# Kernel tuning notes

Hardware: AMD Instinct MI355X
Metric: run time of the kernel (lower is better)

The kernel has to match this reference:

```python
import jax, jax.numpy as jnp
import numpy as np

SIGMA_DIS = 3.0
MAX_LABELS = 33  # label ids in [0, 32]; 0 = background, 1..32 = kernels


def setup_inputs() -> dict:
    key = jax.random.key(0)
    k1, k2 = jax.random.split(key)
    B, C, H, W = 8, 4, 896, 896
    pred = jax.random.normal(k1, (B, C, H, W), dtype=jnp.float32)
    kernels_mask = jnp.ones((B, H, W), dtype=jnp.float32)
    labels = jax.random.randint(k2, (B, H, W), 0, MAX_LABELS, dtype=jnp.int32)
    return {
        "pred_similarities": pred,
        "kernels_mask": kernels_mask,
        "kernel_mask_ndi_labels": labels,
    }


def _disc_loss(pred, labels, sigma):
    # pred: [B, C, H, W], labels: [B, H, W] int
    B, C = pred.shape[0], pred.shape[1]
    p = pred.reshape(B, C, -1)        # [B, C, N]
    lab = labels.reshape(B, -1)       # [B, N]

    # Masks for distinct labels are disjoint, so for a = pred*mask_i/|K_i|,
    # b = pred*mask_j/|K_j|:  ||a - b||_F^2 = s_i + s_j where
    # s_k = sum_{pixels in K_k} sum_c pred^2 / |K_k|^2.
    sq = jnp.sum(p * p, axis=1)       # [B, N]

    def seg(x, l):
        return jax.ops.segment_sum(x, l, num_segments=MAX_LABELS)

    card = jax.vmap(seg)(jnp.ones_like(sq), lab)   # [B, L] pixel counts
    ssq = jax.vmap(seg)(sq, lab)                   # [B, L] sum of squares
    safe_card = jnp.where(card > 0, card, 1.0)
    s = ssq / (safe_card * safe_card)              # [B, L]

    nk = jnp.max(lab, axis=1)                      # [B] num_kernels per image
    ks = jnp.arange(MAX_LABELS)
    valid = (ks[None, :] >= 1) & (ks[None, :] <= nk[:, None]) & (card > 0)  # [B, L]

    # all unordered pairs i < j of valid labels
    pair_mask = (
        valid[:, :, None] & valid[:, None, :] & (ks[:, None] < ks[None, :])[None]
    )  # [B, L, L]
    S = s[:, :, None] + s[:, None, :]
    S_safe = jnp.where(pair_mask, S, 1.0)          # keep sqrt grads finite
    # NOTE: original torch.max(norm, 0)[0] on a 0-d tensor is a dim-reduction
    # over a size-1 view and is an identity, NOT a clamp; replicated faithfully.
    d = sigma - jnp.sqrt(S_safe)
    term = jnp.log(d * d + 1.0)
    per_b = jnp.sum(jnp.where(pair_mask, term, 0.0), axis=(1, 2))  # [B]

    nk_f = nk.astype(per_b.dtype)
    denom = jnp.where(nk > 1, nk_f * (nk_f - 1.0), 1.0)
    loss_b = jnp.where(nk > 1, per_b / denom, 0.0)
    return jnp.sum(loss_b)


def reference(pred_similarities, kernels_mask, kernel_mask_ndi_labels):
    # kernels_mask is reshaped but never used by the original forward math.
    return _disc_loss(pred_similarities, kernel_mask_ndi_labels, SIGMA_DIS)
```

## Files before the change

### kernel.cpp

```cpp
#include <hip/hip_runtime.h>

#define MAXL 33
#define PB 128
#define TPB 128

__global__ __launch_bounds__(TPB, 2) void seg_hist_kernel(
    const float* __restrict__ pred, const int* __restrict__ labels,
    float* __restrict__ partial, int N) {
  const int b = blockIdx.y;
  const int ng = N >> 2;
  __shared__ float sumh[TPB * MAXL];
  __shared__ unsigned cnth[TPB * MAXL];
  __shared__ float xred[2][2][MAXL];
  const int tid = threadIdx.x;

  float* sh = &sumh[tid * MAXL];
  unsigned* ch = &cnth[tid * MAXL];
#pragma unroll
  for (int i = 0; i < MAXL; ++i) {
    sh[i] = 0.f;
    ch[i] = 0u;
  }

  const float4* p = reinterpret_cast<const float4*>(pred) + (size_t)b * 4 * ng;
  const int4* lb = reinterpret_cast<const int4*>(labels) + (size_t)b * ng;
  const int STRIDE = PB * TPB;

  int g = blockIdx.x * TPB + tid;
  float4 c0 = p[g], c1 = p[g + ng], c2 = p[g + 2 * ng], c3 = p[g + 3 * ng];
  int4 l = lb[g];

  while (true) {
    const int gn = g + STRIDE;
    const bool more = gn < ng;
    float4 n0, n1, n2, n3;
    int4 nl;
    if (more) {
      n0 = p[gn];
      n1 = p[gn + ng];
      n2 = p[gn + 2 * ng];
      n3 = p[gn + 3 * ng];
      nl = lb[gn];
    }

    float s0 = c0.x * c0.x + c1.x * c1.x + c2.x * c2.x + c3.x * c3.x;
    float s1 = c0.y * c0.y + c1.y * c1.y + c2.y * c2.y + c3.y * c3.y;
    float s2 = c0.z * c0.z + c1.z * c1.z + c2.z * c2.z + c3.z * c3.z;
    float s3 = c0.w * c0.w + c1.w * c1.w + c2.w * c2.w + c3.w * c3.w;

    const bool e01 = l.x == l.y, e02 = l.x == l.z, e03 = l.x == l.w;
    const bool e12 = l.y == l.z, e13 = l.y == l.w, e23 = l.z == l.w;
    const float w1 = s1 + (e01 ? s0 : 0.f);
    const float w2 = s2 + (e12 ? s1 : 0.f) + (e02 ? s0 : 0.f);
    const float w3 =
        s3 + (e23 ? s2 : 0.f) + (e13 ? s1 : 0.f) + (e03 ? s0 : 0.f);
    const unsigned m1 = 1u + (unsigned)e01;
    const unsigned m2 = 1u + (unsigned)e12 + (unsigned)e02;
    const unsigned m3 = 1u + (unsigned)e23 + (unsigned)e13 + (unsigned)e03;

    const float r0 = sh[l.x], r1 = sh[l.y], r2 = sh[l.z], r3 = sh[l.w];
    const unsigned q0 = ch[l.x], q1 = ch[l.y], q2 = ch[l.z], q3 = ch[l.w];
    sh[l.x] = r0 + s0;
    sh[l.y] = r1 + w1;
    sh[l.z] = r2 + w2;
    sh[l.w] = r3 + w3;
    ch[l.x] = q0 + 1u;
    ch[l.y] = q1 + m1;
    ch[l.z] = q2 + m2;
    ch[l.w] = q3 + m3;

    if (!more) break;
    c0 = n0;
    c1 = n1;
    c2 = n2;
    c3 = n3;
    l = nl;
    g = gn;
  }
  __syncthreads();

  const int wave = tid >> 6;
  const int lane = tid & 63;
  if (lane < MAXL) {
    float fs = 0.f;
    unsigned fc = 0u;
#pragma unroll 8
    for (int u = 0; u < 64; ++u) {
      fs += sumh[(wave * 64 + u) * MAXL + lane];
      fc += cnth[(wave * 64 + u) * MAXL + lane];
    }
    xred[wave][0][lane] = fs;
    xred[wave][1][lane] = (float)fc;
  }
  __syncthreads();
  if (tid < MAXL) {
    partial[(size_t)(b * 2 * MAXL + tid) * PB + blockIdx.x] =
        xred[0][0][tid] + xred[1][0][tid];
    partial[(size_t)(b * 2 * MAXL + MAXL + tid) * PB + blockIdx.x] =
        xred[0][1][tid] + xred[1][1][tid];
  }
}

__global__ __launch_bounds__(512) void reduce_finalize_kernel(
    const float* __restrict__ partial, float* __restrict__ out) {
  __shared__ float red[8 * 2 * MAXL];
  __shared__ float s_val[8 * MAXL];
  __shared__ float s_flag[8 * MAXL];
  __shared__ float s_invden[8];
  __shared__ float s_part[8];
  const int tid = threadIdx.x;
  const int wave = tid >> 6;
  const int lane = tid & 63;

  {
    int slot = tid;
    const float4* row =
        reinterpret_cast<const float4*>(partial) + (size_t)slot * (PB / 4);
    float a0 = 0.f, a1 = 0.f;
#pragma unroll 8
    for (int u = 0; u < PB / 4; u += 2) {
      float4 x = row[u], y = row[u + 1];
      a0 += x.x + x.y + x.z + x.w;
      a1 += y.x + y.y + y.z + y.w;
    }
    if (slot < 8 * 2 * MAXL) red[slot] = a0 + a1;
  }
  if (tid < 8 * 2 * MAXL - 512) {
    int slot = 512 + tid;
    const float4* row =
        reinterpret_cast<const float4*>(partial) + (size_t)slot * (PB / 4);
    float a0 = 0.f, a1 = 0.f;
#pragma unroll 8
    for (int u = 0; u < PB / 4; u += 2) {
      float4 x = row[u], y = row[u + 1];
      a0 += x.x + x.y + x.z + x.w;
      a1 += y.x + y.y + y.z + y.w;
    }
    red[slot] = a0 + a1;
  }
  __syncthreads();

  for (int i = tid; i < 8 * MAXL; i += 512) {
    int b = i / MAXL, l = i - b * MAXL;
    float cnt = red[b * 2 * MAXL + MAXL + l];
    float ssq = red[b * 2 * MAXL + l];
    float safe = cnt > 0.f ? cnt : 1.f;
    s_val[i] = ssq / (safe * safe);
    s_flag[i] = (l >= 1 && cnt > 0.f) ? 1.f : 0.f;
  }
  __syncthreads();
  if (tid < 8) {
    int nk = 0;
    for (int l = MAXL - 1; l >= 0; --l) {
      if (red[tid * 2 * MAXL + MAXL + l] > 0.f) {
        nk = l;
        break;
      }
    }
    s_invden[tid] = (nk > 1) ? 1.f / ((float)nk * ((float)nk - 1.f)) : 0.f;
  }
  __syncthreads();

  float local = 0.f;
  const int total = 8 * MAXL * MAXL;
  for (int idx = tid; idx < total; idx += 512) {
    int b = idx / (MAXL * MAXL);
    int r = idx - b * MAXL * MAXL;
    int i = r / MAXL;
    int j = r - i * MAXL;
    if (i < j && s_flag[b * MAXL + i] != 0.f && s_flag[b * MAXL + j] != 0.f) {
      float S = s_val[b * MAXL + i] + s_val[b * MAXL + j];
      float d = 3.0f - sqrtf(S);
      local += logf(d * d + 1.f) * s_invden[b];
    }
  }
  for (int off = 32; off; off >>= 1) local += __shfl_down(local, off, 64);
  if (lane == 0) s_part[wave] = local;
  __syncthreads();
  if (tid == 0) {
    float tot = 0.f;
    for (int w = 0; w < 8; ++w) tot += s_part[w];
    out[0] = tot;
  }
}

extern "C" void kernel_launch(void* const* d_in, const int* in_sizes, int n_in,
                              void* d_out, int out_size, void* d_ws,
                              size_t ws_size, hipStream_t stream) {
  const float* pred = (const float*)d_in[0];
  const int* labels = (const int*)d_in[2];
  float* out = (float*)d_out;

  const int B = 8;
  const int N = in_sizes[2] / B;

  float* partial = (float*)d_ws;

  dim3 grid(PB, B);
  seg_hist_kernel<<<grid, dim3(TPB), 0, stream>>>(pred, labels, partial, N);
  reduce_finalize_kernel<<<dim3(1), dim3(512), 0, stream>>>(partial, out);
}
```

Baseline: 39.45 us.

## Fuse histogram and finalize kernels via last-block atomic counter, unroll loads for input shape

Merges the reduce/finalize kernel into the histogram kernel: each block writes its partials, bumps a global atomic counter, and the last block to finish performs the cross-block reduction and pairwise loss. The grid-stride loop is replaced by a fixed 12-or-13 iteration schedule with two-deep batched loads, which hardcodes the trip count for N=896*896. This removes one kernel launch at the cost of a memset, threadfences, and a serial tail on one 128-thread block.

```diff
diff --git a/kernel.cpp b/kernel.cpp
--- a/kernel.cpp
+++ b/kernel.cpp
@@ -3,15 +3,22 @@
 #define MAXL 33
 #define PB 128
 #define TPB 128
+#define NBLK (PB * 8)
+#define GSTR (PB * TPB)
 
-__global__ __launch_bounds__(TPB, 2) void seg_hist_kernel(
+__global__ __launch_bounds__(TPB, 2) void disc_loss_fused_kernel(
     const float* __restrict__ pred, const int* __restrict__ labels,
-    float* __restrict__ partial, int N) {
+    float* __restrict__ partial, unsigned* __restrict__ counter,
+    float* __restrict__ out, int N) {
   const int b = blockIdx.y;
   const int ng = N >> 2;
   __shared__ float sumh[TPB * MAXL];
   __shared__ unsigned cnth[TPB * MAXL];
   __shared__ float xred[2][2][MAXL];
+  __shared__ float red[8 * 2 * MAXL];
+  __shared__ float s_invden[8];
+  __shared__ float s_part[2];
+  __shared__ unsigned s_last;
   const int tid = threadIdx.x;
 
   float* sh = &sumh[tid * MAXL];
@@ -24,30 +31,22 @@
 
   const float4* p = reinterpret_cast<const float4*>(pred) + (size_t)b * 4 * ng;
   const int4* lb = reinterpret_cast<const int4*>(labels) + (size_t)b * ng;
-  const int STRIDE = PB * TPB;
+  const int start = blockIdx.x * TPB + tid;
 
-  int g = blockIdx.x * TPB + tid;
-  float4 c0 = p[g], c1 = p[g + ng], c2 = p[g + 2 * ng], c3 = p[g + 3 * ng];
-  int4 l = lb[g];
-
-  while (true) {
-    const int gn = g + STRIDE;
-    const bool more = gn < ng;
-    float4 n0, n1, n2, n3;
-    int4 nl;
-    if (more) {
-      n0 = p[gn];
-      n1 = p[gn + ng];
-      n2 = p[gn + 2 * ng];
-      n3 = p[gn + 3 * ng];
-      nl = lb[gn];
-    }
-
+  auto ld = [&](int g, float4& c0, float4& c1, float4& c2, float4& c3,
+                int4& l) {
+    c0 = p[g];
+    c1 = p[g + ng];
+    c2 = p[g + 2 * ng];
+    c3 = p[g + 3 * ng];
+    l = lb[g];
+  };
+  auto proc = [&](const float4& c0, const float4& c1, const float4& c2,
+                  const float4& c3, const int4& l) {
     float s0 = c0.x * c0.x + c1.x * c1.x + c2.x * c2.x + c3.x * c3.x;
     float s1 = c0.y * c0.y + c1.y * c1.y + c2.y * c2.y + c3.y * c3.y;
     float s2 = c0.z * c0.z + c1.z * c1.z + c2.z * c2.z + c3.z * c3.z;
     float s3 = c0.w * c0.w + c1.w * c1.w + c2.w * c2.w + c3.w * c3.w;
-
     const bool e01 = l.x == l.y, e02 = l.x == l.z, e03 = l.x == l.w;
     const bool e12 = l.y == l.z, e13 = l.y == l.w, e23 = l.z == l.w;
     const float w1 = s1 + (e01 ? s0 : 0.f);
@@ -57,7 +56,6 @@
     const unsigned m1 = 1u + (unsigned)e01;
     const unsigned m2 = 1u + (unsigned)e12 + (unsigned)e02;
     const unsigned m3 = 1u + (unsigned)e23 + (unsigned)e13 + (unsigned)e03;
-
     const float r0 = sh[l.x], r1 = sh[l.y], r2 = sh[l.z], r3 = sh[l.w];
     const unsigned q0 = ch[l.x], q1 = ch[l.y], q2 = ch[l.z], q3 = ch[l.w];
     sh[l.x] = r0 + s0;
@@ -68,15 +66,34 @@
     ch[l.y] = q1 + m1;
     ch[l.z] = q2 + m2;
     ch[l.w] = q3 + m3;
+  };
 
-    if (!more) break;
-    c0 = n0;
-    c1 = n1;
-    c2 = n2;
-    c3 = n3;
-    l = nl;
-    g = gn;
+  const bool has4 = (start + 12 * GSTR) < ng;
+
+  float4 a0, a1, a2, a3, a4, a5, a6, a7;
+  float4 b0, b1, b2, b3, b4, b5, b6, b7;
+  int4 al, al2, bl, bl2;
+
+  ld(start, a0, a1, a2, a3, al);
+  ld(start + GSTR, a4, a5, a6, a7, al2);
+#pragma unroll
+  for (int k = 0; k < 3; ++k) {
+    const int bb = start + (4 * k + 2) * GSTR;
+    ld(bb, b0, b1, b2, b3, bl);
+    ld(bb + GSTR, b4, b5, b6, b7, bl2);
+    proc(a0, a1, a2, a3, al);
+    proc(a4, a5, a6, a7, al2);
+    if (k < 2) {
+      const int ab = start + (4 * k + 4) * GSTR;
+      ld(ab, a0, a1, a2, a3, al);
+      ld(ab + GSTR, a4, a5, a6, a7, al2);
+    } else if (has4) {
+      ld(start + 12 * GSTR, a0, a1, a2, a3, al);
+    }
+    proc(b0, b1, b2, b3, bl);
+    proc(b4, b5, b6, b7, bl2);
   }
+  if (has4) proc(a0, a1, a2, a3, al);
   __syncthreads();
 
   const int wave = tid >> 6;
@@ -99,59 +116,32 @@
     partial[(size_t)(b * 2 * MAXL + MAXL + tid) * PB + blockIdx.x] =
         xred[0][1][tid] + xred[1][1][tid];
   }
-}
+  __syncthreads();
+  __threadfence();
+  if (tid == 0) {
+    unsigned t = atomicAdd(counter, 1u);
+    s_last = (t == NBLK - 1) ? 1u : 0u;
+  }
+  __syncthreads();
+  if (s_last == 0u) return;
 
-__global__ __launch_bounds__(512) void reduce_finalize_kernel(
-    const float* __restrict__ partial, float* __restrict__ out) {
-  __shared__ float red[8 * 2 * MAXL];
-  __shared__ float s_val[8 * MAXL];
-  __shared__ float s_flag[8 * MAXL];
-  __shared__ float s_invden[8];
-  __shared__ float s_part[8];
-  const int tid = threadIdx.x;
-  const int wave = tid >> 6;
-  const int lane = tid & 63;
-
-  {
-    int slot = tid;
+  __threadfence();
+  for (int slot = tid; slot < 8 * 2 * MAXL; slot += TPB) {
     const float4* row =
         reinterpret_cast<const float4*>(partial) + (size_t)slot * (PB / 4);
-    float a0 = 0.f, a1 = 0.f;
+    float acc0 = 0.f, acc1 = 0.f;
 #pragma unroll 8
     for (int u = 0; u < PB / 4; u += 2) {
       float4 x = row[u], y = row[u + 1];
-      a0 += x.x + x.y + x.z + x.w;
-      a1 += y.x + y.y + y.z + y.w;
+      acc0 += x.x + x.y + x.z + x.w;
+      acc1 += y.x + y.y + y.z + y.w;
     }
-    if (slot < 8 * 2 * MAXL) red[slot] = a0 + a1;
-  }
-  if (tid < 8 * 2 * MAXL - 512) {
-    int slot = 512 + tid;
-    const float4* row =
-        reinterpret_cast<const float4*>(partial) + (size_t)slot * (PB / 4);
-    float a0 = 0.f, a1 = 0.f;
-#pragma unroll 8
-    for (int u = 0; u < PB / 4; u += 2) {
-      float4 x = row[u], y = row[u + 1];
-      a0 += x.x + x.y + x.z + x.w;
-      a1 += y.x + y.y + y.z + y.w;
-    }
-    red[slot] = a0 + a1;
-  }
-  __syncthreads();
-
-  for (int i = tid; i < 8 * MAXL; i += 512) {
-    int b = i / MAXL, l = i - b * MAXL;
-    float cnt = red[b * 2 * MAXL + MAXL + l];
-    float ssq = red[b * 2 * MAXL + l];
-    float safe = cnt > 0.f ? cnt : 1.f;
-    s_val[i] = ssq / (safe * safe);
-    s_flag[i] = (l >= 1 && cnt > 0.f) ? 1.f : 0.f;
+    red[slot] = acc0 + acc1;
   }
   __syncthreads();
   if (tid < 8) {
     int nk = 0;
-    for (int l = MAXL - 1; l >= 0; --l) {
+    for (int l = MAXL - 1; l >= 1; --l) {
       if (red[tid * 2 * MAXL + MAXL + l] > 0.f) {
         nk = l;
         break;
@@ -160,28 +150,27 @@
     s_invden[tid] = (nk > 1) ? 1.f / ((float)nk * ((float)nk - 1.f)) : 0.f;
   }
   __syncthreads();
-
   float local = 0.f;
-  const int total = 8 * MAXL * MAXL;
-  for (int idx = tid; idx < total; idx += 512) {
-    int b = idx / (MAXL * MAXL);
-    int r = idx - b * MAXL * MAXL;
+  for (int idx = tid; idx < 8 * MAXL * MAXL; idx += TPB) {
+    int bb = idx / (MAXL * MAXL);
+    int r = idx - bb * MAXL * MAXL;
     int i = r / MAXL;
     int j = r - i * MAXL;
-    if (i < j && s_flag[b * MAXL + i] != 0.f && s_flag[b * MAXL + j] != 0.f) {
-      float S = s_val[b * MAXL + i] + s_val[b * MAXL + j];
-      float d = 3.0f - sqrtf(S);
-      local += logf(d * d + 1.f) * s_invden[b];
+    if (i >= 1 && i < j) {
+      float ci = red[bb * 2 * MAXL + MAXL + i];
+      float cj = red[bb * 2 * MAXL + MAXL + j];
+      if (ci > 0.f && cj > 0.f) {
+        float si = red[bb * 2 * MAXL + i] / (ci * ci);
+        float sj = red[bb * 2 * MAXL + j] / (cj * cj);
+        float d = 3.0f - sqrtf(si + sj);
+        local += logf(d * d + 1.f) * s_invden[bb];
+      }
     }
   }
   for (int off = 32; off; off >>= 1) local += __shfl_down(local, off, 64);
   if (lane == 0) s_part[wave] = local;
   __syncthreads();
-  if (tid == 0) {
-    float tot = 0.f;
-    for (int w = 0; w < 8; ++w) tot += s_part[w];
-    out[0] = tot;
-  }
+  if (tid == 0) out[0] = s_part[0] + s_part[1];
 }
 
 extern "C" void kernel_launch(void* const* d_in, const int* in_sizes, int n_in,
@@ -195,8 +184,10 @@
   const int N = in_sizes[2] / B;
 
   float* partial = (float*)d_ws;
+  unsigned* counter = (unsigned*)((char*)d_ws + 528 * PB * sizeof(float));
+  hipMemsetAsync(counter, 0, sizeof(unsigned), stream);
 
   dim3 grid(PB, B);
-  seg_hist_kernel<<<grid, dim3(TPB), 0, stream>>>(pred, labels, partial, N);
-  reduce_finalize_kernel<<<dim3(1), dim3(512), 0, stream>>>(partial, out);
+  disc_loss_fused_kernel<<<grid, dim3(TPB), 0, stream>>>(pred, labels, partial,
+                                                         counter, out, N);
 }
```

Measured after the change: 116.8 us. +196.0%, slower.
